# Kernel optimization log

Measured on AMD Instinct MI355X. Metric: run time of the kernel, lower is better.

## Reference

```python
import jax, jax.numpy as jnp
import numpy as np

DIM = 1024
NUM_HEADS = 16
HEAD_DIM = DIM // NUM_HEADS
SCALE = HEAD_DIM ** -0.5


def setup_inputs() -> dict:
    key = jax.random.key(0)
    ks = jax.random.split(key, 7)
    B, N, L, C = 2, 1024, 4096, DIM
    s = C ** -0.5
    return {
        "x": jax.random.normal(ks[0], (B, N, C), jnp.float32),
        "y": jax.random.normal(ks[1], (B, L, C), jnp.float32),
        "Wq": jax.random.normal(ks[2], (C, C), jnp.float32) * s,
        "Wk": jax.random.normal(ks[3], (C, C), jnp.float32) * s,
        "Wv": jax.random.normal(ks[4], (C, C), jnp.float32) * s,
        "Wp": jax.random.normal(ks[5], (C, C), jnp.float32) * s,
        "bp": jax.random.normal(ks[6], (C,), jnp.float32) * 0.01,
    }


def reference(x, y, Wq, Wk, Wv, Wp, bp):
    B, N, C = x.shape
    L = y.shape[1]
    H, D = NUM_HEADS, HEAD_DIM
    # torch nn.Linear: out = inp @ W.T
    q = (x @ Wq.T).reshape(B, N, H, D)
    k = (y @ Wk.T).reshape(B, L, H, D)
    v = (y @ Wv.T).reshape(B, L, H, D)
    attn = jnp.einsum("bnhd,blhd->bhnl", q, k)  # [B,H,N,L]
    attn = jax.nn.softmax(SCALE * attn, axis=-1)
    out = jnp.einsum("bhnl,blhd->bnhd", attn, v).reshape(B, N, C)
    return out @ Wp.T + bp
```

## Files before the change

kernel.cpp:

```cpp
#include <hip/hip_runtime.h>
#include <hip/hip_bf16.h>
#include <stdint.h>

typedef __bf16 bf16x8 __attribute__((ext_vector_type(8)));
typedef __bf16 bf16x4 __attribute__((ext_vector_type(4)));
typedef float f32x4 __attribute__((ext_vector_type(4)));

#define MFMA16(a, b, c) __builtin_amdgcn_mfma_f32_16x16x32_bf16((a), (b), (c), 0, 0, 0)
#define SB() __builtin_amdgcn_sched_barrier(0)

__device__ __forceinline__ ushort f2bf(float f) {
  union { float f; uint32_t u; } a; a.f = f;
  uint32_t u = a.u;
  return (ushort)((u + 0x7fffu + ((u >> 16) & 1u)) >> 16);
}

__device__ __forceinline__ void glds16(const void* g, void* l) {
  __builtin_amdgcn_global_load_lds(
      (const __attribute__((address_space(1))) uint32_t*)g,
      (__attribute__((address_space(3))) uint32_t*)l, 16, 0, 0);
}

__global__ __launch_bounds__(256) void cvt_xy(const float* __restrict__ x,
                                              const float* __restrict__ y,
                                              ushort* __restrict__ xb,
                                              ushort* __restrict__ yb) {
  const int bid = blockIdx.x;
  const float* in;
  ushort* out;
  int i;
  if (bid < 2048) { in = x; out = xb; i = bid * 1024 + threadIdx.x * 4; }
  else            { in = y; out = yb; i = (bid - 2048) * 1024 + threadIdx.x * 4; }
  float4 v = *(const float4*)(in + i);
  ushort4 o;
  o.x = f2bf(v.x); o.y = f2bf(v.y); o.z = f2bf(v.z); o.w = f2bf(v.w);
  *(ushort4*)(out + i) = o;
}

__global__ __launch_bounds__(256) void cvt_w(
    const float* __restrict__ a, const float* __restrict__ b,
    const float* __restrict__ c, const float* __restrict__ d,
    ushort* __restrict__ oa, ushort* __restrict__ ob,
    ushort* __restrict__ oc, ushort* __restrict__ od) {
  const int bid = blockIdx.x;
  const int sel = bid >> 10;
  const int i = (bid & 1023) * 1024 + threadIdx.x * 4;
  const float* in = (sel == 0) ? a : (sel == 1) ? b : (sel == 2) ? c : d;
  ushort* out = (sel == 0) ? oa : (sel == 1) ? ob : (sel == 2) ? oc : od;
  float4 v = *(const float4*)(in + i);
  ushort4 o;
  o.x = f2bf(v.x); o.y = f2bf(v.y); o.z = f2bf(v.z); o.w = f2bf(v.w);
  *(ushort4*)(out + i) = o;
}

template <int EPI, int BM, int BN>
__global__ __launch_bounds__(256) void gemm_bt(
    const ushort* __restrict__ A, const ushort* __restrict__ Bw,
    void* __restrict__ Cout, int K, float scale, const float* __restrict__ bias) {
  constexpr int NN = 1024;
  constexpr int WM = BM / 2, WN = BN / 2;
  constexpr int AM = WM / 16, BNF = WN / 16;
  __shared__ ushort ldsA[2][BM * 32];
  __shared__ ushort ldsB[2][BN * 32];
  __shared__ ushort ldsT[(EPI == 1) ? (4 * 64 * 64) : 8];

  const int tid = threadIdx.x;
  const int w = tid >> 6, l = tid & 63;
  const int wm = w >> 1, wn = w & 1;
  const int m0 = blockIdx.x * BM, n0 = blockIdx.y * BN;

  f32x4 acc[AM][BNF] = {};

  const int srow = l >> 2;
  const int schunk = l & 3;

  auto stage = [&](int buf, int kt) {
#pragma unroll
    for (int r = 0; r < BM / 64; ++r) {
      const int rb = r * 64 + w * 16;
      const int row = rb + srow;
      const int j = schunk ^ ((row >> 1) & 3);
      glds16(A + (size_t)(m0 + row) * K + kt + j * 8, (char*)&ldsA[buf][0] + rb * 64);
    }
#pragma unroll
    for (int r = 0; r < BN / 64; ++r) {
      const int rb = r * 64 + w * 16;
      const int row = rb + srow;
      const int j = schunk ^ ((row >> 1) & 3);
      glds16(Bw + (size_t)(n0 + row) * K + kt + j * 8, (char*)&ldsB[buf][0] + rb * 64);
    }
  };

  const int nt = K / 32;
  stage(0, 0);
  asm volatile("s_waitcnt vmcnt(0)" ::: "memory");
  SB(); __builtin_amdgcn_s_barrier(); SB();

  for (int t = 0; t < nt; ++t) {
    const int buf = t & 1;
    if (t + 1 < nt) stage(buf ^ 1, (t + 1) * 32);
    bf16x8 af[AM], bfr[BNF];
#pragma unroll
    for (int a = 0; a < AM; ++a) {
      const int rt = wm * WM + a * 16 + (l & 15);
      const int j = (l >> 4) ^ ((rt >> 1) & 3);
      af[a] = *(const bf16x8*)((const char*)&ldsA[buf][0] + rt * 64 + j * 16);
    }
#pragma unroll
    for (int bx = 0; bx < BNF; ++bx) {
      const int rt = wn * WN + bx * 16 + (l & 15);
      const int j = (l >> 4) ^ ((rt >> 1) & 3);
      bfr[bx] = *(const bf16x8*)((const char*)&ldsB[buf][0] + rt * 64 + j * 16);
    }
#pragma unroll
    for (int am = 0; am < AM; ++am)
#pragma unroll
      for (int bn = 0; bn < BNF; ++bn)
        acc[am][bn] = MFMA16(af[am], bfr[bn], acc[am][bn]);
    if (t + 1 < nt) {
      asm volatile("s_waitcnt vmcnt(0)" ::: "memory");
      SB(); __builtin_amdgcn_s_barrier(); SB();
    }
  }

  if constexpr (EPI == 0) {
#pragma unroll
    for (int am = 0; am < AM; ++am)
#pragma unroll
      for (int bn = 0; bn < BNF; ++bn)
#pragma unroll
        for (int i = 0; i < 4; ++i) {
          const int row = m0 + wm * WM + am * 16 + (l >> 4) * 4 + i;
          const int col = n0 + wn * WN + bn * 16 + (l & 15);
          ((ushort*)Cout)[(size_t)row * NN + col] = f2bf(acc[am][bn][i] * scale);
        }
  } else if constexpr (EPI == 2) {
#pragma unroll
    for (int am = 0; am < AM; ++am)
#pragma unroll
      for (int bn = 0; bn < BNF; ++bn)
#pragma unroll
        for (int i = 0; i < 4; ++i) {
          const int row = m0 + wm * WM + am * 16 + (l >> 4) * 4 + i;
          const int col = n0 + wn * WN + bn * 16 + (l & 15);
          ((float*)Cout)[(size_t)row * NN + col] = acc[am][bn][i] + bias[col];
        }
  } else {
    ushort* tp = ldsT + w * 4096;
#pragma unroll
    for (int am = 0; am < AM; ++am)
#pragma unroll
      for (int bn = 0; bn < BNF; ++bn)
#pragma unroll
        for (int i = 0; i < 4; ++i) {
          const int ml = am * 16 + (l >> 4) * 4 + i;
          const int cl = bn * 16 + (l & 15);
          tp[cl * 64 + ml] = f2bf(acc[am][bn][i]);
        }
    __syncthreads();
#pragma unroll
    for (int it = 0; it < 8; ++it) {
      const int cl = it * 8 + (l >> 3);
      const int mc = l & 7;
      bf16x8 vv = *(const bf16x8*)(tp + cl * 64 + mc * 8);
      const int gcol = n0 + wn * WN + cl;
      const int gm = m0 + wm * WM + mc * 8;
      const int b = gm >> 12;
      const int l_ = gm & 4095;
      const int h = gcol >> 6, d = gcol & 63;
      *(bf16x8*)((ushort*)Cout + (((size_t)b * 16 + h) * 64 + d) * 4096 + l_) = vv;
    }
  }
}

__global__ __launch_bounds__(256) void attn_fused(
    const ushort* __restrict__ qb, const ushort* __restrict__ kb,
    const ushort* __restrict__ vT, ushort* __restrict__ ao) {
  constexpr int H = 16, D = 64, L = 4096, N = 1024, KB = 128;
  __shared__ ushort ldsK[2][KB * 64];
  __shared__ ushort ldsV[2][64 * KB];

  const int tid = threadIdx.x, w = tid >> 6, l = tid & 63;
  const int wg = blockIdx.x;
  const int v = (wg & 7) * 64 + (wg >> 3);
  const int bh = v >> 4;
  const int n0 = (v & 15) * 64;
  const int b = bh >> 4, h = bh & 15;
  const int hq = l >> 4;
  const int m = l & 15;

  bf16x8 qf[2];
  {
    const int qrow = n0 + w * 16 + m;
    const ushort* qp = qb + (((size_t)b * N + qrow) * H + h) * D + hq * 8;
    qf[0] = *(const bf16x8*)qp;
    qf[1] = *(const bf16x8*)(qp + 32);
  }

  f32x4 oacc[4] = {};
  float m_run = -1e30f, l_run = 0.f;

  auto stage = [&](int buf, int l0) {
#pragma unroll
    for (int r = 0; r < 4; ++r) {
      const int rb = (w * 4 + r) * 8;
      const int row = rb + (l >> 3);
      const int sk = (row & 3) + 4 * ((row >> 3) & 1);
      const int j = (l & 7) ^ sk;
      glds16(kb + (((size_t)b * L + l0 + row) * H + h) * D + j * 8,
             (char*)&ldsK[buf][0] + rb * 128);
    }
#pragma unroll
    for (int r = 0; r < 4; ++r) {
      const int rb = (w * 4 + r) * 4;
      const int row = rb + (l >> 4);
      const int j = (l & 15) ^ (row & 15);
      glds16(vT + ((size_t)(b * H + h) * D + row) * L + l0 + j * 8,
             (char*)&ldsV[buf][0] + rb * 256);
    }
  };

  stage(0, 0);

  const int rtl = 8 * (m >> 2) + (m & 3);
  const int skl = (m & 3) + 4 * ((m >> 2) & 1);

  for (int t = 0; t < L / KB; ++t) {
    const int buf = t & 1;
    if (t < L / KB - 1) {
      stage(buf ^ 1, (t + 1) * KB);
      asm volatile("s_waitcnt vmcnt(8)" ::: "memory");
    } else {
      asm volatile("s_waitcnt vmcnt(0)" ::: "memory");
    }
    SB(); __builtin_amdgcn_s_barrier(); SB();

    f32x4 sacc[8] = {};
    __builtin_amdgcn_s_setprio(1);
#pragma unroll
    for (int c = 0; c < 8; ++c) {
      const int rt = 32 * (c >> 1) + 4 * (c & 1) + rtl;
#pragma unroll
      for (int ks = 0; ks < 2; ++ks) {
        const int j = ks * 4 + hq;
        bf16x8 kf = *(const bf16x8*)((const char*)&ldsK[buf][0] + rt * 128 + ((j ^ skl) << 4));
        sacc[c] = MFMA16(kf, qf[ks], sacc[c]);
      }
    }
    __builtin_amdgcn_s_setprio(0);

    float mt = -1e30f;
#pragma unroll
    for (int c = 0; c < 8; ++c)
#pragma unroll
      for (int i = 0; i < 4; ++i) mt = fmaxf(mt, sacc[c][i]);
    mt = fmaxf(mt, __shfl_xor(mt, 16, 64));
    mt = fmaxf(mt, __shfl_xor(mt, 32, 64));
    if (!__all(mt <= m_run + 8.f)) {
      const float mn = fmaxf(m_run, mt);
      const float corr = __builtin_amdgcn_exp2f(m_run - mn);
      float corrO[4];
#pragma unroll
      for (int i = 0; i < 4; ++i) corrO[i] = __shfl(corr, hq * 4 + i, 64);
#pragma unroll
      for (int c = 0; c < 4; ++c)
#pragma unroll
        for (int i = 0; i < 4; ++i) oacc[c][i] *= corrO[i];
      l_run *= corr;
      m_run = mn;
    }
    float rs = 0.f;
#pragma unroll
    for (int c = 0; c < 8; ++c)
#pragma unroll
      for (int i = 0; i < 4; ++i) {
        const float p = __builtin_amdgcn_exp2f(sacc[c][i] - m_run);
        sacc[c][i] = p;
        rs += p;
      }
    rs += __shfl_xor(rs, 16, 64);
    rs += __shfl_xor(rs, 32, 64);
    l_run += rs;

    bf16x8 pf[4];
#pragma unroll
    for (int ks = 0; ks < 4; ++ks)
#pragma unroll
      for (int i = 0; i < 4; ++i) {
        pf[ks][i]     = (__bf16)sacc[2 * ks][i];
        pf[ks][4 + i] = (__bf16)sacc[2 * ks + 1][i];
      }

    __builtin_amdgcn_s_setprio(1);
#pragma unroll
    for (int c = 0; c < 4; ++c) {
      const int rt = c * 16 + m;
#pragma unroll
      for (int ks = 0; ks < 4; ++ks) {
        const int j = ks * 4 + hq;
        bf16x8 vf = *(const bf16x8*)((const char*)&ldsV[buf][0] + rt * 256 + ((j ^ (rt & 15)) << 4));
        oacc[c] = MFMA16(pf[ks], vf, oacc[c]);
      }
    }
    __builtin_amdgcn_s_setprio(0);
    SB(); __builtin_amdgcn_s_barrier(); SB();
  }

  float lr[4];
#pragma unroll
  for (int i = 0; i < 4; ++i) lr[i] = __shfl(l_run, hq * 4 + i, 64);
#pragma unroll
  for (int c = 0; c < 4; ++c)
#pragma unroll
    for (int i = 0; i < 4; ++i) {
      const int n = n0 + w * 16 + hq * 4 + i;
      const int d = c * 16 + m;
      ao[(((size_t)b * N + n) * H + h) * D + d] = f2bf(oacc[c][i] / lr[i]);
    }
}

extern "C" void kernel_launch(void* const* d_in, const int* in_sizes, int n_in,
                              void* d_out, int out_size, void* d_ws, size_t ws_size,
                              hipStream_t stream) {
  const float* x  = (const float*)d_in[0];
  const float* y  = (const float*)d_in[1];
  const float* Wq = (const float*)d_in[2];
  const float* Wk = (const float*)d_in[3];
  const float* Wv = (const float*)d_in[4];
  const float* Wp = (const float*)d_in[5];
  const float* bp = (const float*)d_in[6];
  float* out = (float*)d_out;

  const size_t M1 = 1u << 20;
  ushort* wsb = (ushort*)d_ws;
  ushort* xb  = wsb;
  ushort* yb  = wsb + 2 * M1;
  ushort* wqb = wsb + 10 * M1;
  ushort* wkb = wsb + 11 * M1;
  ushort* wvb = wsb + 12 * M1;
  ushort* wpb = wsb + 13 * M1;
  ushort* qbf = wsb + 14 * M1;
  ushort* kbf = wsb + 16 * M1;
  ushort* vtb = wsb + 24 * M1;
  ushort* aob = wsb + 32 * M1;

  cvt_xy<<<10240, 256, 0, stream>>>(x, y, xb, yb);
  cvt_w<<<4096, 256, 0, stream>>>(Wq, Wk, Wv, Wp, wqb, wkb, wvb, wpb);

  const float qscale = 0.125f * 1.4426950408889634f;
  gemm_bt<0, 64, 64><<<dim3(32, 16), 256, 0, stream>>>(xb, wqb, qbf, 1024, qscale, nullptr);
  gemm_bt<0, 128, 128><<<dim3(64, 8), 256, 0, stream>>>(yb, wkb, kbf, 1024, 1.0f, nullptr);
  gemm_bt<1, 128, 128><<<dim3(64, 8), 256, 0, stream>>>(yb, wvb, vtb, 1024, 1.0f, nullptr);

  attn_fused<<<512, 256, 0, stream>>>(qbf, kbf, vtb, aob);

  gemm_bt<2, 64, 64><<<dim3(32, 16), 256, 0, stream>>>(aob, wpb, out, 1024, 1.0f, bp);
}
```

Before: 250.0 us.

## Split KV tile across waves with all 64 queries per wave, merge in LDS

```diff
diff --git a/kernel.cpp b/kernel.cpp
--- a/kernel.cpp
+++ b/kernel.cpp
@@ -177,8 +177,12 @@
     const ushort* __restrict__ qb, const ushort* __restrict__ kb,
     const ushort* __restrict__ vT, ushort* __restrict__ ao) {
   constexpr int H = 16, D = 64, L = 4096, N = 1024, KB = 128;
-  __shared__ ushort ldsK[2][KB * 64];
-  __shared__ ushort ldsV[2][64 * KB];
+  __shared__ char ldsraw[2 * KB * 64 * 2 + 2 * 64 * KB * 2];
+  __shared__ float ldsM[4][64];
+  __shared__ float ldsL[4][64];
+  ushort* ldsK0 = (ushort*)ldsraw;
+  ushort* ldsV0 = (ushort*)(ldsraw + 2 * KB * 64 * 2);
+  float* ldsO = (float*)ldsraw;
 
   const int tid = threadIdx.x, w = tid >> 6, l = tid & 63;
   const int wg = blockIdx.x;
@@ -189,26 +193,33 @@
   const int hq = l >> 4;
   const int m = l & 15;
 
-  bf16x8 qf[2];
-  {
-    const int qrow = n0 + w * 16 + m;
-    const ushort* qp = qb + (((size_t)b * N + qrow) * H + h) * D + hq * 8;
-    qf[0] = *(const bf16x8*)qp;
-    qf[1] = *(const bf16x8*)(qp + 32);
-  }
-
-  f32x4 oacc[4] = {};
-  float m_run = -1e30f, l_run = 0.f;
+  bf16x8 qf[4][2];
+#pragma unroll
+  for (int qa = 0; qa < 4; ++qa) {
+    const ushort* qp = qb + (((size_t)b * N + n0 + 16 * qa + m) * H + h) * D + hq * 8;
+    qf[qa][0] = *(const bf16x8*)qp;
+    qf[qa][1] = *(const bf16x8*)(qp + 32);
+  }
+
+  f32x4 oacc[4][4] = {};
+  f32x4 lfr[4] = {};
+  float m_run[4];
+#pragma unroll
+  for (int qa = 0; qa < 4; ++qa) m_run[qa] = -1e30f;
+
+  bf16x8 vones;
+#pragma unroll
+  for (int j = 0; j < 8; ++j) vones[j] = (__bf16)1.0f;
 
   auto stage = [&](int buf, int l0) {
 #pragma unroll
     for (int r = 0; r < 4; ++r) {
       const int rb = (w * 4 + r) * 8;
       const int row = rb + (l >> 3);
-      const int sk = (row & 3) + 4 * ((row >> 3) & 1);
+      const int sk = 4 * ((row >> 3) & 1) + (row & 3);
       const int j = (l & 7) ^ sk;
       glds16(kb + (((size_t)b * L + l0 + row) * H + h) * D + j * 8,
-             (char*)&ldsK[buf][0] + rb * 128);
+             (char*)(ldsK0 + buf * KB * 64) + rb * 128);
     }
 #pragma unroll
     for (int r = 0; r < 4; ++r) {
@@ -216,14 +227,14 @@
       const int row = rb + (l >> 4);
       const int j = (l & 15) ^ (row & 15);
       glds16(vT + ((size_t)(b * H + h) * D + row) * L + l0 + j * 8,
-             (char*)&ldsV[buf][0] + rb * 256);
+             (char*)(ldsV0 + buf * 64 * KB) + rb * 256);
     }
   };
 
   stage(0, 0);
 
-  const int rtl = 8 * (m >> 2) + (m & 3);
-  const int skl = (m & 3) + 4 * ((m >> 2) & 1);
+  const int rtl = 32 * w + 8 * (m >> 2) + (m & 3);
+  const int sk = 4 * ((m >> 2) & 1) + (m & 3);
 
   for (int t = 0; t < L / KB; ++t) {
     const int buf = t & 1;
@@ -235,88 +246,119 @@
     }
     SB(); __builtin_amdgcn_s_barrier(); SB();
 
-    f32x4 sacc[8] = {};
+    const char* kbase = (const char*)(ldsK0 + buf * KB * 64);
+    const char* vbase = (const char*)(ldsV0 + buf * 64 * KB);
+
+    f32x4 sacc[2][4] = {};
     __builtin_amdgcn_s_setprio(1);
 #pragma unroll
-    for (int c = 0; c < 8; ++c) {
-      const int rt = 32 * (c >> 1) + 4 * (c & 1) + rtl;
+    for (int la = 0; la < 2; ++la) {
+      const int rt = rtl + 4 * la;
 #pragma unroll
       for (int ks = 0; ks < 2; ++ks) {
-        const int j = ks * 4 + hq;
-        bf16x8 kf = *(const bf16x8*)((const char*)&ldsK[buf][0] + rt * 128 + ((j ^ skl) << 4));
-        sacc[c] = MFMA16(kf, qf[ks], sacc[c]);
+        bf16x8 kf = *(const bf16x8*)(kbase + rt * 128 + (((ks * 4 + hq) ^ sk) << 4));
+#pragma unroll
+        for (int qa = 0; qa < 4; ++qa)
+          sacc[la][qa] = MFMA16(kf, qf[qa][ks], sacc[la][qa]);
       }
     }
     __builtin_amdgcn_s_setprio(0);
 
-    float mt = -1e30f;
-#pragma unroll
-    for (int c = 0; c < 8; ++c)
-#pragma unroll
-      for (int i = 0; i < 4; ++i) mt = fmaxf(mt, sacc[c][i]);
-    mt = fmaxf(mt, __shfl_xor(mt, 16, 64));
-    mt = fmaxf(mt, __shfl_xor(mt, 32, 64));
-    if (!__all(mt <= m_run + 8.f)) {
-      const float mn = fmaxf(m_run, mt);
-      const float corr = __builtin_amdgcn_exp2f(m_run - mn);
-      float corrO[4];
-#pragma unroll
-      for (int i = 0; i < 4; ++i) corrO[i] = __shfl(corr, hq * 4 + i, 64);
-#pragma unroll
-      for (int c = 0; c < 4; ++c)
-#pragma unroll
-        for (int i = 0; i < 4; ++i) oacc[c][i] *= corrO[i];
-      l_run *= corr;
-      m_run = mn;
-    }
-    float rs = 0.f;
-#pragma unroll
-    for (int c = 0; c < 8; ++c)
+    float mt[4];
+#pragma unroll
+    for (int qa = 0; qa < 4; ++qa) {
+      float a0 = fmaxf(fmaxf(sacc[0][qa][0], sacc[0][qa][1]),
+                       fmaxf(sacc[0][qa][2], sacc[0][qa][3]));
+      float a1 = fmaxf(fmaxf(sacc[1][qa][0], sacc[1][qa][1]),
+                       fmaxf(sacc[1][qa][2], sacc[1][qa][3]));
+      float mq = fmaxf(a0, a1);
+      mq = fmaxf(mq, __shfl_xor(mq, 16, 64));
+      mq = fmaxf(mq, __shfl_xor(mq, 32, 64));
+      mt[qa] = mq;
+    }
+    bool ok = (mt[0] <= m_run[0] + 8.f) && (mt[1] <= m_run[1] + 8.f) &&
+              (mt[2] <= m_run[2] + 8.f) && (mt[3] <= m_run[3] + 8.f);
+    if (!__all(ok)) {
+#pragma unroll
+      for (int qa = 0; qa < 4; ++qa) {
+        const float mn = fmaxf(m_run[qa], mt[qa]);
+        const float corr = __builtin_amdgcn_exp2f(m_run[qa] - mn);
+        m_run[qa] = mn;
+        f32x4 co;
+#pragma unroll
+        for (int i = 0; i < 4; ++i) co[i] = __shfl(corr, hq * 4 + i, 64);
+#pragma unroll
+        for (int c = 0; c < 4; ++c) oacc[qa][c] *= co;
+        lfr[qa] *= co;
+      }
+    }
+    bf16x8 pf[4];
+#pragma unroll
+    for (int qa = 0; qa < 4; ++qa)
 #pragma unroll
       for (int i = 0; i < 4; ++i) {
-        const float p = __builtin_amdgcn_exp2f(sacc[c][i] - m_run);
-        sacc[c][i] = p;
-        rs += p;
-      }
-    rs += __shfl_xor(rs, 16, 64);
-    rs += __shfl_xor(rs, 32, 64);
-    l_run += rs;
-
-    bf16x8 pf[4];
-#pragma unroll
-    for (int ks = 0; ks < 4; ++ks)
-#pragma unroll
-      for (int i = 0; i < 4; ++i) {
-        pf[ks][i]     = (__bf16)sacc[2 * ks][i];
-        pf[ks][4 + i] = (__bf16)sacc[2 * ks + 1][i];
+        pf[qa][i]     = (__bf16)__builtin_amdgcn_exp2f(sacc[0][qa][i] - m_run[qa]);
+        pf[qa][4 + i] = (__bf16)__builtin_amdgcn_exp2f(sacc[1][qa][i] - m_run[qa]);
       }
 
     __builtin_amdgcn_s_setprio(1);
 #pragma unroll
     for (int c = 0; c < 4; ++c) {
       const int rt = c * 16 + m;
-#pragma unroll
-      for (int ks = 0; ks < 4; ++ks) {
-        const int j = ks * 4 + hq;
-        bf16x8 vf = *(const bf16x8*)((const char*)&ldsV[buf][0] + rt * 256 + ((j ^ (rt & 15)) << 4));
-        oacc[c] = MFMA16(pf[ks], vf, oacc[c]);
-      }
-    }
+      bf16x8 vf = *(const bf16x8*)(vbase + rt * 256 + ((((4 * w + hq)) ^ (rt & 15)) << 4));
+#pragma unroll
+      for (int qa = 0; qa < 4; ++qa)
+        oacc[qa][c] = MFMA16(pf[qa], vf, oacc[qa][c]);
+    }
+#pragma unroll
+    for (int qa = 0; qa < 4; ++qa) lfr[qa] = MFMA16(pf[qa], vones, lfr[qa]);
     __builtin_amdgcn_s_setprio(0);
     SB(); __builtin_amdgcn_s_barrier(); SB();
   }
 
-  float lr[4];
-#pragma unroll
-  for (int i = 0; i < 4; ++i) lr[i] = __shfl(l_run, hq * 4 + i, 64);
-#pragma unroll
-  for (int c = 0; c < 4; ++c)
-#pragma unroll
-    for (int i = 0; i < 4; ++i) {
-      const int n = n0 + w * 16 + hq * 4 + i;
-      const int d = c * 16 + m;
-      ao[(((size_t)b * N + n) * H + h) * D + d] = f2bf(oacc[c][i] / lr[i]);
-    }
+#pragma unroll
+  for (int qa = 0; qa < 4; ++qa)
+#pragma unroll
+    for (int c = 0; c < 4; ++c)
+#pragma unroll
+      for (int i = 0; i < 4; ++i)
+        ldsO[w * 4096 + (16 * qa + 4 * hq + i) * 64 + 16 * c + m] = oacc[qa][c][i];
+  if (hq == 0) {
+#pragma unroll
+    for (int qa = 0; qa < 4; ++qa) ldsM[w][16 * qa + m] = m_run[qa];
+  }
+  if (m == 0) {
+#pragma unroll
+    for (int qa = 0; qa < 4; ++qa)
+#pragma unroll
+      for (int i = 0; i < 4; ++i) ldsL[w][16 * qa + 4 * hq + i] = lfr[qa][i];
+  }
+  __syncthreads();
+
+  const int q = 16 * w + m;
+  const float Mx = fmaxf(fmaxf(ldsM[0][q], ldsM[1][q]), fmaxf(ldsM[2][q], ldsM[3][q]));
+  f32x4 av[4] = {};
+  float Lt = 0.f;
+#pragma unroll
+  for (int wp = 0; wp < 4; ++wp) {
+    const float sc = __builtin_amdgcn_exp2f(ldsM[wp][q] - Mx);
+    Lt += ldsL[wp][q] * sc;
+    const float* op = ldsO + wp * 4096 + q * 64 + hq * 16;
+#pragma unroll
+    for (int g = 0; g < 4; ++g) {
+      f32x4 t4 = *(const f32x4*)(op + g * 4);
+      av[g] += t4 * sc;
+    }
+  }
+  const float inv = 1.0f / Lt;
+  ushort* aop = ao + (((size_t)b * N + n0 + q) * H + h) * D + hq * 16;
+#pragma unroll
+  for (int g = 0; g < 4; ++g) {
+    ushort4 o4;
+    o4.x = f2bf(av[g][0] * inv); o4.y = f2bf(av[g][1] * inv);
+    o4.z = f2bf(av[g][2] * inv); o4.w = f2bf(av[g][3] * inv);
+    *(ushort4*)(aop + g * 4) = o4;
+  }
 }
 
 extern "C" void kernel_launch(void* const* d_in, const int* in_sizes, int n_in,
```

After: 294.7 us. +17.9%, slower.
